# Performance work log

Measured on AMD Instinct MI355X. Metric: run time of the kernel, lower is better.

## Reference

```python
import jax, jax.numpy as jnp
import numpy as np

NV, NC, E, D = 100000, 400000, 1600000, 128

def _mlp2(x, w1, b1, w2, b2):
    # Linear->ReLU->Linear->ReLU (weights stored [in, out])
    return jax.nn.relu(jax.nn.relu(x @ w1 + b1) @ w2 + b2)

def setup_inputs() -> dict:
    key = jax.random.key(0)
    ks = jax.random.split(key, 16)
    s = 1.0 / np.sqrt(D)
    return {
        "hv": jax.random.normal(ks[0], (NV, D), jnp.float32),
        "hc": jax.random.normal(ks[1], (NC, D), jnp.float32),
        "row_v": jax.random.randint(ks[2], (E,), 0, NV, jnp.int32),
        "col_v": jax.random.randint(ks[3], (E,), 0, 2 * NC, jnp.int32),
        "row_c": jax.random.randint(ks[4], (E,), 0, NC, jnp.int32),
        "col_c": jax.random.randint(ks[5], (E,), 0, 2 * NV, jnp.int32),
        # message MLPs: order [fmv_pos, fmv_neg, fmc_pos, fmc_neg]
        "mw1": jax.random.normal(ks[6], (4, D, D), jnp.float32) * s,
        "mb1": jax.random.normal(ks[7], (4, D), jnp.float32) * s,
        "mw2": jax.random.normal(ks[8], (4, D, D), jnp.float32) * s,
        "mb2": jax.random.normal(ks[9], (4, D), jnp.float32) * s,
        # update MLPs: order [fuv, fuc]; first layer takes concat(h, m) -> 2D in
        "uw1": jax.random.normal(ks[10], (2, 2 * D, D), jnp.float32) * s,
        "ub1": jax.random.normal(ks[11], (2, D), jnp.float32) * s,
        "uw2": jax.random.normal(ks[12], (2, D, D), jnp.float32) * s,
        "ub2": jax.random.normal(ks[13], (2, D), jnp.float32) * s,
    }

def reference(hv, hc, row_v, col_v, row_c, col_c,
              mw1, mb1, mw2, mb2, uw1, ub1, uw2, ub2):
    nv, nc = hv.shape[0], hc.shape[0]
    # message: transform clause feats with pos/neg MLPs, concat rows, spmm via gather+segment_sum
    zv = jnp.concatenate([
        _mlp2(hc, mw1[0], mb1[0], mw2[0], mb2[0]),  # fmv_pos(hc)
        _mlp2(hc, mw1[1], mb1[1], mw2[1], mb2[1]),  # fmv_neg(hc)
    ], axis=0)                                       # [2*NC, D]
    mv = jax.ops.segment_sum(zv[col_v], row_v, num_segments=nv)  # spmm(vadj, zv)
    zc = jnp.concatenate([
        _mlp2(hv, mw1[2], mb1[2], mw2[2], mb2[2]),  # fmc_pos(hv)
        _mlp2(hv, mw1[3], mb1[3], mw2[3], mb2[3]),  # fmc_neg(hv)
    ], axis=0)                                       # [2*NV, D]
    mc = jax.ops.segment_sum(zc[col_c], row_c, num_segments=nc)  # spmm(cadj, zc)
    # update: concat(h, m) -> MLP
    hv_new = _mlp2(jnp.concatenate([hv, mv], axis=1), uw1[0], ub1[0], uw2[0], ub2[0])
    hc_new = _mlp2(jnp.concatenate([hc, mc], axis=1), uw1[1], ub1[1], uw2[1], ub2[1])
    return (hv_new, hc_new)
```

## Files before the change

kernel.cpp:

```cpp
#include <hip/hip_runtime.h>
#include <hip/hip_bf16.h>

#define NVV 100000
#define NCC 400000
#define NEE 1600000

typedef short short8 __attribute__((ext_vector_type(8)));
typedef short short4v __attribute__((ext_vector_type(4)));
typedef float f32x4 __attribute__((ext_vector_type(4)));
typedef unsigned int u32x2 __attribute__((ext_vector_type(2)));
typedef unsigned int u32x4 __attribute__((ext_vector_type(4)));

__device__ __forceinline__ float b2f(short s) {
    unsigned int u = ((unsigned int)(unsigned short)s) << 16;
    return __builtin_bit_cast(float, u);
}
__device__ __forceinline__ short f2b(float f) {
    __hip_bfloat16 h = __float2bfloat16(f);
    return __builtin_bit_cast(short, h);
}
__device__ __forceinline__ unsigned int cvtpk(float a, float b) {
    unsigned int r;
    asm("v_cvt_pk_bf16_f32 %0, %1, %2" : "=v"(r) : "v"(a), "v"(b));
    return r;
}
__device__ __forceinline__ short8 gload16(const short* p) {
    short8 d;
    asm volatile("global_load_dwordx4 %0, %1, off" : "=v"(d) : "v"(p));
    return d;
}
#define SB0() __builtin_amdgcn_sched_barrier(0)

__global__ __launch_bounds__(256)
void prep_all(const float* __restrict__ mw1, const float* __restrict__ mw2,
              const float* __restrict__ uw1, const float* __restrict__ uw2,
              short* __restrict__ wt_m1, short* __restrict__ wt_m2,
              short* __restrict__ wt_u1, short* __restrict__ wt_u2)
{
    int e = blockIdx.x * 256 + threadIdx.x;
    const float* W; short* WT; int K; int idx;
    if (e < 65536)        { W = mw1; WT = wt_m1; K = 128; idx = e; }
    else if (e < 131072)  { W = mw2; WT = wt_m2; K = 128; idx = e - 65536; }
    else if (e < 196608)  { W = uw1; WT = wt_u1; K = 256; idx = e - 131072; }
    else if (e < 229376)  { W = uw2; WT = wt_u2; K = 128; idx = e - 196608; }
    else return;
    int mk = idx >> 7, n = idx & 127;
    int mi = mk / K, k = mk - mi * K;
    WT[(size_t)mi * K * 128 + (size_t)n * K + k] = f2b(W[idx]);
}

__global__ __launch_bounds__(256)
void to_bf16_2(const float* __restrict__ hv, const float* __restrict__ hc,
               short* __restrict__ hvb, short* __restrict__ hcb)
{
    const long nv = (long)NVV * 128;
    const long nc = (long)NCC * 128;
    long i0 = ((long)blockIdx.x * 256 + threadIdx.x) * 8;
    long stride = (long)gridDim.x * 256 * 8;
    for (long i = i0; i < nv + nc; i += stride) {
        const float* in; short* outp; long j;
        if (i < nv) { in = hv; outp = hvb; j = i; }
        else        { in = hc; outp = hcb; j = i - nv; }
        f32x4 a = *(const f32x4*)(in + j);
        f32x4 b = *(const f32x4*)(in + j + 4);
        u32x4 o;
        o[0] = cvtpk(a[0], a[1]);
        o[1] = cvtpk(a[2], a[3]);
        o[2] = cvtpk(b[0], b[1]);
        o[3] = cvtpk(b[2], b[3]);
        *(u32x4*)(outp + j) = o;
    }
}

template<int NW>
__global__ __launch_bounds__(NW * 64, 1)
void mlp2_msg_all(const short* __restrict__ hcb, const short* __restrict__ hvb,
                  const short* __restrict__ WT1, const float* __restrict__ B1a,
                  const short* __restrict__ WT2, const float* __restrict__ B2a,
                  short* __restrict__ zv, short* __restrict__ zc, int splitC)
{
    constexpr int BM = NW * 32;
    constexpr int NT = NW * 64;
    __shared__ short sW1[128 * 136];
    __shared__ short sW2[128 * 136];
    __shared__ short sH[BM * 136];

    const int tid = threadIdx.x;
    const int lane = tid & 63;
    const int w = tid >> 6;
    const int p = lane & 15;
    const int q = lane >> 4;

    int b = blockIdx.x;
    const short* X; short* z; int M, c0, cstr, set;
    if (b < splitC) {
        set = b & 1; X = hcb; z = zv + (size_t)set * NCC * 128;
        M = NCC; c0 = b >> 1; cstr = splitC >> 1;
    } else {
        int bb = b - splitC;
        set = 2 + (bb & 1); X = hvb; z = zc + (size_t)(bb & 1) * NVV * 128;
        M = NVV; c0 = bb >> 1; cstr = (gridDim.x - splitC) >> 1;
    }
    const int nChunks = (M + BM - 1) / BM;

    const short* w1g = WT1 + set * 16384;
    const short* w2g = WT2 + set * 16384;
    const float* b1g = B1a + set * 128;
    const float* b2g = B2a + set * 128;

    for (int e = tid * 8; e < 128 * 128; e += NT * 8) {
        int n = e >> 7, k = e & 127;
        *(short8*)(sW1 + n * 136 + k) = *(const short8*)(w1g + e);
        *(short8*)(sW2 + n * 136 + k) = *(const short8*)(w2g + e);
    }
    __syncthreads();

    if (c0 >= nChunks) return;

    short8 xfA[2][4], xfB[2][4];

    auto issueX = [&](short8 (&xf)[2][4], int c) {
        long base = (long)c * BM + w * 32;
        #pragma unroll
        for (int t = 0; t < 2; ++t) {
            long m = base + t * 16 + p;
            if (m > (long)M - 1) m = (long)M - 1;
            const short* src = X + m * 128 + q * 8;
            #pragma unroll
            for (int kk = 0; kk < 4; ++kk)
                xf[t][kk] = gload16(src + kk * 32);
        }
        SB0();
    };

    auto computeStore = [&](const short8 (&xf)[2][4], int c) {
        long base = (long)c * BM + w * 32;
        f32x4 acc[8][2];
        #pragma unroll
        for (int cc = 0; cc < 8; ++cc)
            #pragma unroll
            for (int t = 0; t < 2; ++t)
                acc[cc][t] = (f32x4){0.f, 0.f, 0.f, 0.f};

        #pragma unroll
        for (int kk = 0; kk < 4; ++kk) {
            short8 af[8];
            #pragma unroll
            for (int cc = 0; cc < 8; ++cc)
                af[cc] = *(const short8*)(sW1 + (cc * 16 + p) * 136 + kk * 32 + q * 8);
            #pragma unroll
            for (int cc = 0; cc < 8; ++cc)
                #pragma unroll
                for (int t = 0; t < 2; ++t)
                    acc[cc][t] = __builtin_amdgcn_mfma_f32_16x16x32_bf16(af[cc], xf[t][kk], acc[cc][t], 0, 0, 0);
        }

        #pragma unroll
        for (int cc = 0; cc < 8; ++cc) {
            f32x4 bb = *(const f32x4*)(b1g + cc * 16 + q * 4);
            #pragma unroll
            for (int t = 0; t < 2; ++t) {
                u32x2 u;
                u[0] = cvtpk(fmaxf(acc[cc][t][0] + bb[0], 0.f), fmaxf(acc[cc][t][1] + bb[1], 0.f));
                u[1] = cvtpk(fmaxf(acc[cc][t][2] + bb[2], 0.f), fmaxf(acc[cc][t][3] + bb[3], 0.f));
                *(u32x2*)(sH + (w * 32 + t * 16 + p) * 136 + cc * 16 + q * 4) = u;
            }
        }
        asm volatile("s_waitcnt lgkmcnt(0)" ::: "memory");

        f32x4 acc2[8][2];
        #pragma unroll
        for (int cc = 0; cc < 8; ++cc)
            #pragma unroll
            for (int t = 0; t < 2; ++t)
                acc2[cc][t] = (f32x4){0.f, 0.f, 0.f, 0.f};

        #pragma unroll
        for (int kk = 0; kk < 4; ++kk) {
            short8 af[8], bfr[2];
            #pragma unroll
            for (int cc = 0; cc < 8; ++cc)
                af[cc] = *(const short8*)(sW2 + (cc * 16 + p) * 136 + kk * 32 + q * 8);
            #pragma unroll
            for (int t = 0; t < 2; ++t)
                bfr[t] = *(const short8*)(sH + (w * 32 + t * 16 + p) * 136 + kk * 32 + q * 8);
            #pragma unroll
            for (int cc = 0; cc < 8; ++cc)
                #pragma unroll
                for (int t = 0; t < 2; ++t)
                    acc2[cc][t] = __builtin_amdgcn_mfma_f32_16x16x32_bf16(af[cc], bfr[t], acc2[cc][t], 0, 0, 0);
        }

        #pragma unroll
        for (int cc = 0; cc < 8; ++cc) {
            f32x4 bb = *(const f32x4*)(b2g + cc * 16 + q * 4);
            #pragma unroll
            for (int t = 0; t < 2; ++t) {
                long m = base + t * 16 + p;
                if (m < M) {
                    u32x2 u;
                    u[0] = cvtpk(fmaxf(acc2[cc][t][0] + bb[0], 0.f), fmaxf(acc2[cc][t][1] + bb[1], 0.f));
                    u[1] = cvtpk(fmaxf(acc2[cc][t][2] + bb[2], 0.f), fmaxf(acc2[cc][t][3] + bb[3], 0.f));
                    *(u32x2*)(z + m * 128 + cc * 16 + q * 4) = u;
                }
            }
        }
    };

    int c = c0;
    issueX(xfA, c);
    asm volatile("s_waitcnt vmcnt(0)" ::: "memory");
    SB0();
    while (true) {
        {
            bool hn = (c + cstr < nChunks);
            if (hn) issueX(xfB, c + cstr);
            computeStore(xfA, c);
            c += cstr;
            if (!hn) return;
            asm volatile("s_waitcnt vmcnt(16)" ::: "memory");
            SB0();
        }
        {
            bool hn = (c + cstr < nChunks);
            if (hn) issueX(xfA, c + cstr);
            computeStore(xfB, c);
            c += cstr;
            if (!hn) return;
            asm volatile("s_waitcnt vmcnt(16)" ::: "memory");
            SB0();
        }
    }
}

template<int NW>
__global__ __launch_bounds__(NW * 64, 1)
void mlp2_upd_all(const short* __restrict__ hvb, const short* __restrict__ hcb,
                  const short* __restrict__ mv, const short* __restrict__ mc,
                  const short* __restrict__ wt_u1, const float* __restrict__ ub1,
                  const short* __restrict__ wt_u2, const float* __restrict__ ub2,
                  float* __restrict__ out, int splitV)
{
    constexpr int BM = NW * 32;
    constexpr int NT = NW * 64;
    __shared__ short sW1[128 * 264];
    __shared__ short sW2[128 * 136];
    __shared__ short sH[BM * 136];

    const int tid = threadIdx.x;
    const int lane = tid & 63;
    const int w = tid >> 6;
    const int p = lane & 15;
    const int q = lane >> 4;

    int b = blockIdx.x;
    const short *X, *X2; float* O; int M, c0, cstr, set;
    if (b < splitV) {
        set = 0; X = hvb; X2 = mv; O = out; M = NVV; c0 = b; cstr = splitV;
    } else {
        set = 1; X = hcb; X2 = mc; O = out + (size_t)NVV * 128; M = NCC;
        c0 = b - splitV; cstr = gridDim.x - splitV;
    }
    const int nChunks = (M + BM - 1) / BM;

    const short* W1T = wt_u1 + set * 32768;
    const short* W2T = wt_u2 + set * 16384;
    const float* B1 = ub1 + set * 128;
    const float* B2 = ub2 + set * 128;

    for (int e = tid * 8; e < 128 * 256; e += NT * 8) {
        int n = e >> 8, k = e & 255;
        *(short8*)(sW1 + n * 264 + k) = *(const short8*)(W1T + e);
    }
    for (int e = tid * 8; e < 128 * 128; e += NT * 8) {
        int n = e >> 7, k = e & 127;
        *(short8*)(sW2 + n * 136 + k) = *(const short8*)(W2T + e);
    }
    __syncthreads();

    if (c0 >= nChunks) return;

    short8 hA[2][4], hB[2][4], mr[2][4];

    auto issueH = [&](short8 (&h)[2][4], int c) {
        long base = (long)c * BM + w * 32;
        #pragma unroll
        for (int t = 0; t < 2; ++t) {
            long m = base + t * 16 + p;
            if (m > (long)M - 1) m = (long)M - 1;
            const short* s1 = X + m * 128 + q * 8;
            #pragma unroll
            for (int kk = 0; kk < 4; ++kk)
                h[t][kk] = gload16(s1 + kk * 32);
        }
        SB0();
    };
    auto issueM = [&](int c) {
        long base = (long)c * BM + w * 32;
        #pragma unroll
        for (int t = 0; t < 2; ++t) {
            long m = base + t * 16 + p;
            if (m > (long)M - 1) m = (long)M - 1;
            const short* s2 = X2 + m * 128 + q * 8;
            #pragma unroll
            for (int kk = 0; kk < 4; ++kk)
                mr[t][kk] = gload16(s2 + kk * 32);
        }
        SB0();
    };

    auto body = [&](const short8 (&h)[2][4], int c, bool hn, int cn) {
        long base = (long)c * BM + w * 32;
        f32x4 acc[8][2];
        #pragma unroll
        for (int cc = 0; cc < 8; ++cc)
            #pragma unroll
            for (int t = 0; t < 2; ++t)
                acc[cc][t] = (f32x4){0.f, 0.f, 0.f, 0.f};

        #pragma unroll
        for (int kk = 0; kk < 8; ++kk) {
            short8 af[8];
            #pragma unroll
            for (int cc = 0; cc < 8; ++cc)
                af[cc] = *(const short8*)(sW1 + (cc * 16 + p) * 264 + kk * 32 + q * 8);
            #pragma unroll
            for (int cc = 0; cc < 8; ++cc)
                #pragma unroll
                for (int t = 0; t < 2; ++t) {
                    short8 xcur = (kk < 4) ? h[t][kk] : mr[t][kk - 4];
                    acc[cc][t] = __builtin_amdgcn_mfma_f32_16x16x32_bf16(af[cc], xcur, acc[cc][t], 0, 0, 0);
                }
        }

        if (hn) issueM(cn);

        #pragma unroll
        for (int cc = 0; cc < 8; ++cc) {
            f32x4 bb = *(const f32x4*)(B1 + cc * 16 + q * 4);
            #pragma unroll
            for (int t = 0; t < 2; ++t) {
                u32x2 u;
                u[0] = cvtpk(fmaxf(acc[cc][t][0] + bb[0], 0.f), fmaxf(acc[cc][t][1] + bb[1], 0.f));
                u[1] = cvtpk(fmaxf(acc[cc][t][2] + bb[2], 0.f), fmaxf(acc[cc][t][3] + bb[3], 0.f));
                *(u32x2*)(sH + (w * 32 + t * 16 + p) * 136 + cc * 16 + q * 4) = u;
            }
        }
        asm volatile("s_waitcnt lgkmcnt(0)" ::: "memory");

        f32x4 acc2[8][2];
        #pragma unroll
        for (int cc = 0; cc < 8; ++cc)
            #pragma unroll
            for (int t = 0; t < 2; ++t)
                acc2[cc][t] = (f32x4){0.f, 0.f, 0.f, 0.f};

        #pragma unroll
        for (int kk = 0; kk < 4; ++kk) {
            short8 af[8], bfr[2];
            #pragma unroll
            for (int cc = 0; cc < 8; ++cc)
                af[cc] = *(const short8*)(sW2 + (cc * 16 + p) * 136 + kk * 32 + q * 8);
            #pragma unroll
            for (int t = 0; t < 2; ++t)
                bfr[t] = *(const short8*)(sH + (w * 32 + t * 16 + p) * 136 + kk * 32 + q * 8);
            #pragma unroll
            for (int cc = 0; cc < 8; ++cc)
                #pragma unroll
                for (int t = 0; t < 2; ++t)
                    acc2[cc][t] = __builtin_amdgcn_mfma_f32_16x16x32_bf16(af[cc], bfr[t], acc2[cc][t], 0, 0, 0);
        }

        #pragma unroll
        for (int cc = 0; cc < 8; ++cc) {
            f32x4 bb = *(const f32x4*)(B2 + cc * 16 + q * 4);
            #pragma unroll
            for (int t = 0; t < 2; ++t) {
                long m = base + t * 16 + p;
                if (m < M) {
                    f32x4 fv;
                    #pragma unroll
                    for (int i = 0; i < 4; ++i)
                        fv[i] = fmaxf(acc2[cc][t][i] + bb[i], 0.f);
                    *(f32x4*)(O + m * 128 + cc * 16 + q * 4) = fv;
                }
            }
        }
    };

    int c = c0;
    issueH(hA, c);
    issueM(c);
    asm volatile("s_waitcnt vmcnt(0)" ::: "memory");
    SB0();
    while (true) {
        {
            bool hn = (c + cstr < nChunks);
            if (hn) issueH(hB, c + cstr);
            body(hA, c, hn, c + cstr);
            c += cstr;
            if (!hn) return;
            asm volatile("s_waitcnt vmcnt(16)" ::: "memory");
            SB0();
        }
        {
            bool hn = (c + cstr < nChunks);
            if (hn) issueH(hA, c + cstr);
            body(hB, c, hn, c + cstr);
            c += cstr;
            if (!hn) return;
            asm volatile("s_waitcnt vmcnt(16)" ::: "memory");
            SB0();
        }
    }
}


__global__ __launch_bounds__(256)
void hist2(const int* __restrict__ row_v, const int* __restrict__ row_c,
           int* __restrict__ cnt_v, int* __restrict__ cnt_c)
{
    int e = blockIdx.x * 256 + threadIdx.x;
    if (e < NEE) atomicAdd(&cnt_v[row_v[e]], 1);
    else if (e < 2 * NEE) atomicAdd(&cnt_c[row_c[e - NEE]], 1);
}

__global__ __launch_bounds__(256)
void seg_reduce2(const int* __restrict__ cnt_v, const int* __restrict__ cnt_c,
                 int* __restrict__ bsum_v, int* __restrict__ bsum_c, int Bv)
{
    __shared__ int s[256];
    int b = blockIdx.x, t = threadIdx.x;
    const int* counts; int* bsum; int N; int bb;
    if (b < Bv) { counts = cnt_v; bsum = bsum_v; N = NVV; bb = b; }
    else        { counts = cnt_c; bsum = bsum_c; N = NCC; bb = b - Bv; }
    int base = bb * 512;
    int v = 0;
    if (base + t < N) v += counts[base + t];
    if (base + 256 + t < N) v += counts[base + 256 + t];
    s[t] = v;
    __syncthreads();
    for (int off = 128; off > 0; off >>= 1) {
        if (t < off) s[t] += s[t + off];
        __syncthreads();
    }
    if (t == 0) bsum[bb] = s[0];
}

__global__ __launch_bounds__(1024)
void scan_bsum2(int* __restrict__ bsum_v, int* __restrict__ bsum_c, int Bv, int Bc)
{
    __shared__ int s[1024];
    int* bsum = (blockIdx.x == 0) ? bsum_v : bsum_c;
    int B = (blockIdx.x == 0) ? Bv : Bc;
    int t = threadIdx.x;
    s[t] = (t < B) ? bsum[t] : 0;
    __syncthreads();
    for (int off = 1; off < 1024; off <<= 1) {
        int v = (t >= off) ? s[t - off] : 0;
        __syncthreads();
        s[t] += v;
        __syncthreads();
    }
    if (t < B) bsum[t] = (t == 0) ? 0 : s[t - 1];
}

__global__ __launch_bounds__(512)
void scan_final2(const int* __restrict__ cnt_v, const int* __restrict__ cnt_c,
                 const int* __restrict__ bsum_v, const int* __restrict__ bsum_c,
                 int* __restrict__ offs_v, int* __restrict__ offs_c, int Bv)
{
    __shared__ int s[512];
    int b = blockIdx.x, t = threadIdx.x;
    const int* counts; const int* bsum; int* offs; int N; int bb;
    if (b < Bv) { counts = cnt_v; bsum = bsum_v; offs = offs_v; N = NVV; bb = b; }
    else        { counts = cnt_c; bsum = bsum_c; offs = offs_c; N = NCC; bb = b - Bv; }
    int idx = bb * 512 + t;
    int c = (idx < N) ? counts[idx] : 0;
    s[t] = c;
    __syncthreads();
    for (int off = 1; off < 512; off <<= 1) {
        int v = (t >= off) ? s[t - off] : 0;
        __syncthreads();
        s[t] += v;
        __syncthreads();
    }
    if (idx < N) offs[idx] = bsum[bb] + s[t] - c;
    if (idx == N - 1) offs[N] = bsum[bb] + s[t];
}

__global__ __launch_bounds__(256)
void csr_fill2(const int* __restrict__ row_v, const int* __restrict__ col_v,
               const int* __restrict__ row_c, const int* __restrict__ col_c,
               const int* __restrict__ offs_v, const int* __restrict__ offs_c,
               int* __restrict__ cur_v, int* __restrict__ cur_c,
               int* __restrict__ edge_v, int* __restrict__ edge_c)
{
    int e = blockIdx.x * 256 + threadIdx.x;
    if (e < NEE) {
        int r = row_v[e];
        int pos = offs_v[r] + atomicAdd(&cur_v[r], 1);
        edge_v[pos] = col_v[e];
    } else if (e < 2 * NEE) {
        int ee = e - NEE;
        int r = row_c[ee];
        int pos = offs_c[r] + atomicAdd(&cur_c[r], 1);
        edge_c[pos] = col_c[ee];
    }
}

__global__ __launch_bounds__(256)
void csr_gather_all(const short* __restrict__ zv, const short* __restrict__ zc,
                    const int* __restrict__ offs_v, const int* __restrict__ edge_v,
                    const int* __restrict__ offs_c, const int* __restrict__ edge_c,
                    short* __restrict__ mv, short* __restrict__ mc)
{
    int wid = (int)((blockIdx.x * 256 + threadIdx.x) >> 6);
    int lane = threadIdx.x & 63;
    int sub = lane >> 4;
    int sl = lane & 15;
    int row = wid * 4 + sub;
    if (row >= NVV + NCC) return;

    const short* z; const int* offs; const int* ec; short* md; int r;
    if (row < NVV) { z = zv; offs = offs_v; ec = edge_v; md = mv; r = row; }
    else           { z = zc; offs = offs_c; ec = edge_c; md = mc; r = row - NVV; }

    int beg = offs[r], end = offs[r + 1];

    float a[8];
    #pragma unroll
    for (int i = 0; i < 8; ++i) a[i] = 0.f;

    int j = beg;
    for (; j + 3 < end; j += 4) {
        int c0 = ec[j], c1 = ec[j + 1], c2 = ec[j + 2], c3 = ec[j + 3];
        short8 v0 = *(const short8*)(z + (long)c0 * 128 + sl * 8);
        short8 v1 = *(const short8*)(z + (long)c1 * 128 + sl * 8);
        short8 v2 = *(const short8*)(z + (long)c2 * 128 + sl * 8);
        short8 v3 = *(const short8*)(z + (long)c3 * 128 + sl * 8);
        #pragma unroll
        for (int i = 0; i < 8; ++i)
            a[i] += (b2f(v0[i]) + b2f(v1[i])) + (b2f(v2[i]) + b2f(v3[i]));
    }
    for (; j < end; ++j) {
        int c = ec[j];
        short8 v = *(const short8*)(z + (long)c * 128 + sl * 8);
        #pragma unroll
        for (int i = 0; i < 8; ++i) a[i] += b2f(v[i]);
    }

    u32x4 o;
    o[0] = cvtpk(a[0], a[1]);
    o[1] = cvtpk(a[2], a[3]);
    o[2] = cvtpk(a[4], a[5]);
    o[3] = cvtpk(a[6], a[7]);
    *(u32x4*)(md + (long)r * 128 + sl * 8) = o;
}

extern "C" void kernel_launch(void* const* d_in, const int* in_sizes, int n_in,
                              void* d_out, int out_size, void* d_ws, size_t ws_size,
                              hipStream_t stream)
{
    const float* hv   = (const float*)d_in[0];
    const float* hc   = (const float*)d_in[1];
    const int* row_v  = (const int*)d_in[2];
    const int* col_v  = (const int*)d_in[3];
    const int* row_c  = (const int*)d_in[4];
    const int* col_c  = (const int*)d_in[5];
    const float* mw1  = (const float*)d_in[6];
    const float* mb1  = (const float*)d_in[7];
    const float* mw2  = (const float*)d_in[8];
    const float* mb2  = (const float*)d_in[9];
    const float* uw1  = (const float*)d_in[10];
    const float* ub1  = (const float*)d_in[11];
    const float* uw2  = (const float*)d_in[12];
    const float* ub2  = (const float*)d_in[13];
    float* out = (float*)d_out;

    short* zv = (short*)d_ws;
    short* zc = zv + (size_t)2 * NCC * 128;
    short* mv = zc + (size_t)2 * NVV * 128;
    short* mc = mv + (size_t)NVV * 128;
    short* wt_m1 = mc + (size_t)NCC * 128;
    short* wt_m2 = wt_m1 + 4 * 16384;
    short* wt_u1 = wt_m2 + 4 * 16384;
    short* wt_u2 = wt_u1 + 2 * 32768;
    short* hvb = wt_u2 + 2 * 16384;
    short* hcb = hvb + (size_t)NVV * 128;
    int* edge_v = (int*)(hcb + (size_t)NCC * 128);
    int* edge_c = edge_v + NEE;
    int* offs_v = edge_c + NEE;
    int* offs_c = offs_v + (NVV + 1);
    int* cnt_v  = offs_c + (NCC + 1);
    int* cnt_c  = cnt_v + NVV;
    int* bsum_v = cnt_c + NCC;
    int* bsum_c = bsum_v + 1024;

    const int Bv = (NVV + 511) / 512;
    const int Bc = (NCC + 511) / 512;

    prep_all<<<(229376 + 255) / 256, 256, 0, stream>>>(
        mw1, mw2, uw1, uw2, wt_m1, wt_m2, wt_u1, wt_u2);
    to_bf16_2<<<2048, 256, 0, stream>>>(hv, hc, hvb, hcb);

    hipMemsetAsync(cnt_v, 0, (NVV + NCC) * sizeof(int), stream);
    hist2<<<(2 * NEE + 255) / 256, 256, 0, stream>>>(row_v, row_c, cnt_v, cnt_c);
    seg_reduce2<<<Bv + Bc, 256, 0, stream>>>(cnt_v, cnt_c, bsum_v, bsum_c, Bv);
    scan_bsum2<<<2, 1024, 0, stream>>>(bsum_v, bsum_c, Bv, Bc);
    scan_final2<<<Bv + Bc, 512, 0, stream>>>(cnt_v, cnt_c, bsum_v, bsum_c, offs_v, offs_c, Bv);
    hipMemsetAsync(cnt_v, 0, (NVV + NCC) * sizeof(int), stream);
    csr_fill2<<<(2 * NEE + 255) / 256, 256, 0, stream>>>(
        row_v, col_v, row_c, col_c, offs_v, offs_c, cnt_v, cnt_c, edge_v, edge_c);

    mlp2_msg_all<8><<<256, 512, 0, stream>>>(
        hcb, hvb, wt_m1, mb1, wt_m2, mb2, zv, zc, 204);

    csr_gather_all<<<((NVV + NCC) / 4 + 3) / 4, 256, 0, stream>>>(
        zv, zc, offs_v, edge_v, offs_c, edge_c, mv, mc);

    mlp2_upd_all<6><<<256, 384, 0, stream>>>(
        hvb, hcb, mv, mc, wt_u1, ub1, wt_u2, ub2, out, 51);
}
```

Measured before the change: 1.157 ms.

## Build CSR via two-pass bucketed scatter to localize atomics and writes

Replaces the single-pass CSR fill, which did random per-row atomics and scattered writes, with two passes. The first pass bins edges into coarse row buckets (64 rows for variables, 256 for clauses) and writes packed (col,row) pairs. The second pass has one block per bucket place each edge into its final row slot, so the atomics and writes stay within a small region. This is meant to cut cache misses and atomic contention during CSR construction, at the cost of an extra kernel and about 25 MB of extra intermediate traffic.

```diff
diff --git a/kernel.cpp b/kernel.cpp
--- a/kernel.cpp
+++ b/kernel.cpp
@@ -4,6 +4,8 @@
 #define NVV 100000
 #define NCC 400000
 #define NEE 1600000
+#define NBV ((NVV + 63) >> 6)
+#define NBC ((NCC + 255) >> 8)
 
 typedef short short8 __attribute__((ext_vector_type(8)));
 typedef short short4v __attribute__((ext_vector_type(4)));
@@ -490,22 +492,50 @@
 }
 
 __global__ __launch_bounds__(256)
-void csr_fill2(const int* __restrict__ row_v, const int* __restrict__ col_v,
+void bin_fill2(const int* __restrict__ row_v, const int* __restrict__ col_v,
                const int* __restrict__ row_c, const int* __restrict__ col_c,
                const int* __restrict__ offs_v, const int* __restrict__ offs_c,
-               int* __restrict__ cur_v, int* __restrict__ cur_c,
-               int* __restrict__ edge_v, int* __restrict__ edge_c)
+               int* __restrict__ bcur_v, int* __restrict__ bcur_c,
+               long* __restrict__ pr_v, long* __restrict__ pr_c)
 {
     int e = blockIdx.x * 256 + threadIdx.x;
     if (e < NEE) {
-        int r = row_v[e];
-        int pos = offs_v[r] + atomicAdd(&cur_v[r], 1);
-        edge_v[pos] = col_v[e];
+        int r = row_v[e], c = col_v[e];
+        int b = r >> 6;
+        int pos = offs_v[b << 6] + atomicAdd(&bcur_v[b], 1);
+        pr_v[pos] = ((long)c << 32) | (unsigned int)r;
     } else if (e < 2 * NEE) {
         int ee = e - NEE;
-        int r = row_c[ee];
-        int pos = offs_c[r] + atomicAdd(&cur_c[r], 1);
-        edge_c[pos] = col_c[ee];
+        int r = row_c[ee], c = col_c[ee];
+        int b = r >> 8;
+        int pos = offs_c[b << 8] + atomicAdd(&bcur_c[b], 1);
+        pr_c[pos] = ((long)c << 32) | (unsigned int)r;
+    }
+}
+
+__global__ __launch_bounds__(64)
+void bucket_fill2(const long* __restrict__ pr_v, const long* __restrict__ pr_c,
+                  const int* __restrict__ offs_v, const int* __restrict__ offs_c,
+                  int* __restrict__ cur_v, int* __restrict__ cur_c,
+                  int* __restrict__ edge_v, int* __restrict__ edge_c)
+{
+    int b = blockIdx.x;
+    const long* pr; const int* offs; int* cur; int* edge; int r0, r1;
+    if (b < NBV) {
+        pr = pr_v; offs = offs_v; cur = cur_v; edge = edge_v;
+        r0 = b << 6; r1 = min((b + 1) << 6, NVV);
+    } else {
+        int bb = b - NBV;
+        pr = pr_c; offs = offs_c; cur = cur_c; edge = edge_c;
+        r0 = bb << 8; r1 = min((bb + 1) << 8, NCC);
+    }
+    int beg = offs[r0], end = offs[r1];
+    for (int i = beg + (int)threadIdx.x; i < end; i += 64) {
+        long pc = pr[i];
+        int r = (int)(pc & 0xffffffffL);
+        int c = (int)(pc >> 32);
+        int dst = offs[r] + atomicAdd(&cur[r], 1);
+        edge[dst] = c;
     }
 }
 
@@ -588,13 +618,17 @@
     short* wt_u2 = wt_u1 + 2 * 32768;
     short* hvb = wt_u2 + 2 * 16384;
     short* hcb = hvb + (size_t)NVV * 128;
-    int* edge_v = (int*)(hcb + (size_t)NCC * 128);
+    long* pr_v = (long*)(hcb + (size_t)NCC * 128);
+    long* pr_c = pr_v + NEE;
+    int* edge_v = (int*)(pr_c + NEE);
     int* edge_c = edge_v + NEE;
     int* offs_v = edge_c + NEE;
     int* offs_c = offs_v + (NVV + 1);
     int* cnt_v  = offs_c + (NCC + 1);
     int* cnt_c  = cnt_v + NVV;
-    int* bsum_v = cnt_c + NCC;
+    int* bcur_v = cnt_c + NCC;
+    int* bcur_c = bcur_v + NBV;
+    int* bsum_v = bcur_c + NBC;
     int* bsum_c = bsum_v + 1024;
 
     const int Bv = (NVV + 511) / 512;
@@ -609,9 +643,11 @@
     seg_reduce2<<<Bv + Bc, 256, 0, stream>>>(cnt_v, cnt_c, bsum_v, bsum_c, Bv);
     scan_bsum2<<<2, 1024, 0, stream>>>(bsum_v, bsum_c, Bv, Bc);
     scan_final2<<<Bv + Bc, 512, 0, stream>>>(cnt_v, cnt_c, bsum_v, bsum_c, offs_v, offs_c, Bv);
-    hipMemsetAsync(cnt_v, 0, (NVV + NCC) * sizeof(int), stream);
-    csr_fill2<<<(2 * NEE + 255) / 256, 256, 0, stream>>>(
-        row_v, col_v, row_c, col_c, offs_v, offs_c, cnt_v, cnt_c, edge_v, edge_c);
+    hipMemsetAsync(cnt_v, 0, (NVV + NCC + NBV + NBC) * sizeof(int), stream);
+    bin_fill2<<<(2 * NEE + 255) / 256, 256, 0, stream>>>(
+        row_v, col_v, row_c, col_c, offs_v, offs_c, bcur_v, bcur_c, pr_v, pr_c);
+    bucket_fill2<<<NBV + NBC, 64, 0, stream>>>(
+        pr_v, pr_c, offs_v, offs_c, cnt_v, cnt_c, edge_v, edge_c);
 
     mlp2_msg_all<8><<<256, 512, 0, stream>>>(
         hcb, hvb, wt_m1, mb1, wt_m2, mb2, zv, zc, 204);
```

After: 1.469 ms. 1.27x slower.

## Partition histogram and CSR fill atomics by XCD-owned row ranges

Applied to the files above, without the earlier changes.

Rewrites the histogram and CSR-fill kernels so that blockIdx&7 (the XCD under round-robin dispatch) owns one eighth of the row space. Each block group scans every edge but only does atomics for rows in its own range, so atomics on a given counter stay within one XCD's L2 and avoid cross-XCD coherence traffic. In exchange each edge's row index is read eight times, and the grids shrink to 1024 persistent-style blocks.

```diff
diff --git a/kernel.cpp b/kernel.cpp
--- a/kernel.cpp
+++ b/kernel.cpp
@@ -415,14 +415,22 @@
     }
 }
 
-
 __global__ __launch_bounds__(256)
-void hist2(const int* __restrict__ row_v, const int* __restrict__ row_c,
-           int* __restrict__ cnt_v, int* __restrict__ cnt_c)
-{
-    int e = blockIdx.x * 256 + threadIdx.x;
-    if (e < NEE) atomicAdd(&cnt_v[row_v[e]], 1);
-    else if (e < 2 * NEE) atomicAdd(&cnt_c[row_c[e - NEE]], 1);
+void hist_xcd(const int* __restrict__ row_v, const int* __restrict__ row_c,
+              int* __restrict__ cnt_v, int* __restrict__ cnt_c)
+{
+    const int g = blockIdx.x & 7;
+    const int bg = blockIdx.x >> 3, nbg = gridDim.x >> 3;
+    const int r0 = g * (NVV / 8), r1 = r0 + NVV / 8;
+    for (int e = bg * 256 + threadIdx.x; e < NEE; e += nbg * 256) {
+        int r = row_v[e];
+        if (r >= r0 && r < r1) atomicAdd(&cnt_v[r], 1);
+    }
+    const int s0 = g * (NCC / 8), s1 = s0 + NCC / 8;
+    for (int e = bg * 256 + threadIdx.x; e < NEE; e += nbg * 256) {
+        int r = row_c[e];
+        if (r >= s0 && r < s1) atomicAdd(&cnt_c[r], 1);
+    }
 }
 
 __global__ __launch_bounds__(256)
@@ -490,22 +498,29 @@
 }
 
 __global__ __launch_bounds__(256)
-void csr_fill2(const int* __restrict__ row_v, const int* __restrict__ col_v,
-               const int* __restrict__ row_c, const int* __restrict__ col_c,
-               const int* __restrict__ offs_v, const int* __restrict__ offs_c,
-               int* __restrict__ cur_v, int* __restrict__ cur_c,
-               int* __restrict__ edge_v, int* __restrict__ edge_c)
-{
-    int e = blockIdx.x * 256 + threadIdx.x;
-    if (e < NEE) {
+void csr_fill_xcd(const int* __restrict__ row_v, const int* __restrict__ col_v,
+                  const int* __restrict__ row_c, const int* __restrict__ col_c,
+                  const int* __restrict__ offs_v, const int* __restrict__ offs_c,
+                  int* __restrict__ cur_v, int* __restrict__ cur_c,
+                  int* __restrict__ edge_v, int* __restrict__ edge_c)
+{
+    const int g = blockIdx.x & 7;
+    const int bg = blockIdx.x >> 3, nbg = gridDim.x >> 3;
+    const int r0 = g * (NVV / 8), r1 = r0 + NVV / 8;
+    for (int e = bg * 256 + threadIdx.x; e < NEE; e += nbg * 256) {
         int r = row_v[e];
-        int pos = offs_v[r] + atomicAdd(&cur_v[r], 1);
-        edge_v[pos] = col_v[e];
-    } else if (e < 2 * NEE) {
-        int ee = e - NEE;
-        int r = row_c[ee];
-        int pos = offs_c[r] + atomicAdd(&cur_c[r], 1);
-        edge_c[pos] = col_c[ee];
+        if (r >= r0 && r < r1) {
+            int pos = offs_v[r] + atomicAdd(&cur_v[r], 1);
+            edge_v[pos] = col_v[e];
+        }
+    }
+    const int s0 = g * (NCC / 8), s1 = s0 + NCC / 8;
+    for (int e = bg * 256 + threadIdx.x; e < NEE; e += nbg * 256) {
+        int r = row_c[e];
+        if (r >= s0 && r < s1) {
+            int pos = offs_c[r] + atomicAdd(&cur_c[r], 1);
+            edge_c[pos] = col_c[e];
+        }
     }
 }
 
@@ -605,12 +620,12 @@
     to_bf16_2<<<2048, 256, 0, stream>>>(hv, hc, hvb, hcb);
 
     hipMemsetAsync(cnt_v, 0, (NVV + NCC) * sizeof(int), stream);
-    hist2<<<(2 * NEE + 255) / 256, 256, 0, stream>>>(row_v, row_c, cnt_v, cnt_c);
+    hist_xcd<<<1024, 256, 0, stream>>>(row_v, row_c, cnt_v, cnt_c);
     seg_reduce2<<<Bv + Bc, 256, 0, stream>>>(cnt_v, cnt_c, bsum_v, bsum_c, Bv);
     scan_bsum2<<<2, 1024, 0, stream>>>(bsum_v, bsum_c, Bv, Bc);
     scan_final2<<<Bv + Bc, 512, 0, stream>>>(cnt_v, cnt_c, bsum_v, bsum_c, offs_v, offs_c, Bv);
     hipMemsetAsync(cnt_v, 0, (NVV + NCC) * sizeof(int), stream);
-    csr_fill2<<<(2 * NEE + 255) / 256, 256, 0, stream>>>(
+    csr_fill_xcd<<<1024, 256, 0, stream>>>(
         row_v, col_v, row_c, col_c, offs_v, offs_c, cnt_v, cnt_c, edge_v, edge_c);
 
     mlp2_msg_all<8><<<256, 512, 0, stream>>>(
```

After: 1.144 ms. About the same (-1.1%).
